# Kernel optimization log

Hardware: AMD Instinct MI355X
Metric: run time of the kernel (lower is better)

The kernel has to match this reference:

```python
import jax, jax.numpy as jnp
import numpy as np

T, B, I, H = 512, 64, 256, 512

def setup_inputs() -> dict:
    key = jax.random.key(0)
    ks = jax.random.split(key, 5)
    s = 0.1  # matches uniform(-0.1, 0.1) init scale
    return {
        "x": jax.random.normal(ks[0], (T, B, I), dtype=jnp.float32),
        "weight_ih": jax.random.uniform(ks[1], (H, I), dtype=jnp.float32, minval=-s, maxval=s),
        "weight_hh": jax.random.uniform(ks[2], (H, H), dtype=jnp.float32, minval=-s, maxval=s),
        "bias_ih": jax.random.uniform(ks[3], (H,), dtype=jnp.float32, minval=-s, maxval=s),
        "bias_hh": jax.random.uniform(ks[4], (H,), dtype=jnp.float32, minval=-s, maxval=s),
    }

def reference(x, weight_ih, weight_hh, bias_ih, bias_hh):
    # Precompute input contribution for all timesteps in one big GEMM: [T,B,H]
    xw = jnp.einsum('tbi,hi->tbh', x, weight_ih) + bias_ih + bias_hh
    h0 = jnp.zeros((x.shape[1], weight_hh.shape[0]), dtype=x.dtype)

    def step(h, xw_t):
        h = jax.nn.relu(xw_t + h @ weight_hh.T)
        return h, h

    h_final, output = jax.lax.scan(step, h0, xw)
    return output, h_final
```

## Files before the change

### kernel.cpp

```cpp
#include <hip/hip_runtime.h>

#define T_DIM 512
#define B_DIM 64
#define I_DIM 256
#define H_DIM 512
#define BH_DIM (B_DIM * H_DIM)


typedef float f32x4_t __attribute__((ext_vector_type(4)));

__device__ __forceinline__ float4 nt_load4(const float4* p) {
  f32x4_t v = __builtin_nontemporal_load((const f32x4_t*)p);
  return make_float4(v.x, v.y, v.z, v.w);
}

__global__ __launch_bounds__(512, 2) void rnn_fused(
    const float* __restrict__ x, const float* __restrict__ wih,
    const float* __restrict__ whh, const float* __restrict__ bih,
    const float* __restrict__ bhh, float* __restrict__ out,
    unsigned long long* __restrict__ stage) {
  __shared__ __align__(16) float4 wihs4[128 * 64];
  __shared__ __align__(16) float hbuf[2][H_DIM];
  __shared__ __align__(16) float4 xbuf4[3 * 64];

  const int b   = blockIdx.x & 63;
  const int rb  = blockIdx.x >> 6;
  const int tid = threadIdx.x;
  const int rg  = tid >> 4;
  const int cg  = tid & 15;
  const int j0  = rb * 128 + rg * 4;

  const int pj = (tid < rb * 128) ? tid : tid + 128;

  float4 w[4][8];
#pragma unroll
  for (int r = 0; r < 4; r++) {
    const float4* wr = (const float4*)(whh + (size_t)(j0 + r) * H_DIM);
#pragma unroll
    for (int i = 0; i < 8; i++) w[r][i] = wr[i * 16 + cg];
  }

  {
    const float4* wg = (const float4*)(wih + (size_t)rb * 128 * I_DIM);
#pragma unroll
    for (int q = 0; q < 16; q++) {
      const int idx = q * 512 + tid;
      wihs4[idx] = wg[idx];
    }
  }

  const float4* xg = (const float4*)x;
  if (tid < 64) {
    xbuf4[0 * 64 + tid] = nt_load4(&xg[((size_t)0 * B_DIM + b) * 64 + tid]);
    xbuf4[1 * 64 + tid] = nt_load4(&xg[((size_t)1 * B_DIM + b) * 64 + tid]);
  }

  float bias = 0.f;
  if (cg < 4) bias = bih[j0 + cg] + bhh[j0 + cg];

  float* __restrict__ outb = out + (size_t)b * H_DIM;
  unsigned long long* __restrict__ stg0 = stage + (size_t)b * H_DIM;
  unsigned long long* __restrict__ stg1 = stage + (size_t)(64 + b) * H_DIM;

  __syncthreads();

  float hlast = 0.f;

  {
    float b0 = 0.f, b1 = 0.f, b2 = 0.f, b3 = 0.f;
    const float4* xb = &xbuf4[0];
    const float4* wr = &wihs4[(rg * 4) * 64];
#pragma unroll
    for (int i = 0; i < 4; i++) {
      const float4 xv = xb[i * 16 + cg];
      const float4 q0 = wr[0 * 64 + i * 16 + cg];
      const float4 q1 = wr[1 * 64 + i * 16 + cg];
      const float4 q2 = wr[2 * 64 + i * 16 + cg];
      const float4 q3 = wr[3 * 64 + i * 16 + cg];
      b0 = fmaf(q0.x, xv.x, b0); b0 = fmaf(q0.y, xv.y, b0);
      b0 = fmaf(q0.z, xv.z, b0); b0 = fmaf(q0.w, xv.w, b0);
      b1 = fmaf(q1.x, xv.x, b1); b1 = fmaf(q1.y, xv.y, b1);
      b1 = fmaf(q1.z, xv.z, b1); b1 = fmaf(q1.w, xv.w, b1);
      b2 = fmaf(q2.x, xv.x, b2); b2 = fmaf(q2.y, xv.y, b2);
      b2 = fmaf(q2.z, xv.z, b2); b2 = fmaf(q2.w, xv.w, b2);
      b3 = fmaf(q3.x, xv.x, b3); b3 = fmaf(q3.y, xv.y, b3);
      b3 = fmaf(q3.z, xv.z, b3); b3 = fmaf(q3.w, xv.w, b3);
    }
#pragma unroll
    for (int m = 1; m <= 8; m <<= 1) {
      b0 += __shfl_xor(b0, m, 64);
      b1 += __shfl_xor(b1, m, 64);
      b2 += __shfl_xor(b2, m, 64);
      b3 += __shfl_xor(b3, m, 64);
    }
    if (cg < 4) {
      const float acc = (cg == 0) ? b0 : (cg == 1) ? b1 : (cg == 2) ? b2 : b3;
      const float h = fmaxf(acc + bias, 0.f);
      const int j = j0 + cg;
      union { float f; unsigned int u; } cv; cv.f = h;
      __hip_atomic_store(&stg0[j], (unsigned long long)cv.u,
                         __ATOMIC_RELAXED, __HIP_MEMORY_SCOPE_AGENT);
      __builtin_nontemporal_store(h, &outb[j]);
      hbuf[0][j] = h;
      hlast = h;
    }
    if (tid < 64) {
      xbuf4[2 * 64 + tid] = nt_load4(&xg[((size_t)2 * B_DIM + b) * 64 + tid]);
    }
  }

  for (int t = 1; t < T_DIM; t++) {
    const int p = (t - 1) & 1;
    float* hb = hbuf[p];
    float* o_t = outb + (size_t)t * BH_DIM;

    float b0 = 0.f, b1 = 0.f, b2 = 0.f, b3 = 0.f;
    {
      const float4* xb = &xbuf4[(t % 3) * 64];
      const float4* wr = &wihs4[(rg * 4) * 64];
#pragma unroll
      for (int i = 0; i < 4; i++) {
        const float4 xv = xb[i * 16 + cg];
        const float4 q0 = wr[0 * 64 + i * 16 + cg];
        const float4 q1 = wr[1 * 64 + i * 16 + cg];
        const float4 q2 = wr[2 * 64 + i * 16 + cg];
        const float4 q3 = wr[3 * 64 + i * 16 + cg];
        b0 = fmaf(q0.x, xv.x, b0); b0 = fmaf(q0.y, xv.y, b0);
        b0 = fmaf(q0.z, xv.z, b0); b0 = fmaf(q0.w, xv.w, b0);
        b1 = fmaf(q1.x, xv.x, b1); b1 = fmaf(q1.y, xv.y, b1);
        b1 = fmaf(q1.z, xv.z, b1); b1 = fmaf(q1.w, xv.w, b1);
        b2 = fmaf(q2.x, xv.x, b2); b2 = fmaf(q2.y, xv.y, b2);
        b2 = fmaf(q2.z, xv.z, b2); b2 = fmaf(q2.w, xv.w, b2);
        b3 = fmaf(q3.x, xv.x, b3); b3 = fmaf(q3.y, xv.y, b3);
        b3 = fmaf(q3.z, xv.z, b3); b3 = fmaf(q3.w, xv.w, b3);
      }
    }

    float4 xpf = make_float4(0.f, 0.f, 0.f, 0.f);
    const bool do_pf = (tid < 64) && (t + 2 < T_DIM);
    if (do_pf) xpf = nt_load4(&xg[((size_t)(t + 2) * B_DIM + b) * 64 + tid]);

    if (tid < 384) {
      unsigned long long* slot = (p ? stg1 : stg0) + pj;
      const unsigned int want = (unsigned int)(t - 1);
      unsigned long long v;
      do {
        v = __hip_atomic_load(slot, __ATOMIC_RELAXED, __HIP_MEMORY_SCOPE_AGENT);
      } while ((unsigned int)(v >> 32) != want);
      union { unsigned int u; float f; } cv; cv.u = (unsigned int)v;
      hb[pj] = cv.f;
    }

    __syncthreads();

    if (do_pf) xbuf4[((t + 2) % 3) * 64 + tid] = xpf;

    float a0 = b0, a1 = b1, a2 = b2, a3 = b3;
#pragma unroll
    for (int i = 0; i < 8; i++) {
      const float4 hv = ((const float4*)hb)[i * 16 + cg];
      a0 = fmaf(w[0][i].x, hv.x, a0); a0 = fmaf(w[0][i].y, hv.y, a0);
      a0 = fmaf(w[0][i].z, hv.z, a0); a0 = fmaf(w[0][i].w, hv.w, a0);
      a1 = fmaf(w[1][i].x, hv.x, a1); a1 = fmaf(w[1][i].y, hv.y, a1);
      a1 = fmaf(w[1][i].z, hv.z, a1); a1 = fmaf(w[1][i].w, hv.w, a1);
      a2 = fmaf(w[2][i].x, hv.x, a2); a2 = fmaf(w[2][i].y, hv.y, a2);
      a2 = fmaf(w[2][i].z, hv.z, a2); a2 = fmaf(w[2][i].w, hv.w, a2);
      a3 = fmaf(w[3][i].x, hv.x, a3); a3 = fmaf(w[3][i].y, hv.y, a3);
      a3 = fmaf(w[3][i].z, hv.z, a3); a3 = fmaf(w[3][i].w, hv.w, a3);
    }
#pragma unroll
    for (int m = 1; m <= 8; m <<= 1) {
      a0 += __shfl_xor(a0, m, 64);
      a1 += __shfl_xor(a1, m, 64);
      a2 += __shfl_xor(a2, m, 64);
      a3 += __shfl_xor(a3, m, 64);
    }

    if (cg < 4) {
      const float acc = (cg == 0) ? a0 : (cg == 1) ? a1 : (cg == 2) ? a2 : a3;
      const float h = fmaxf(acc + bias, 0.f);
      const int j = j0 + cg;
      union { float f; unsigned int u; } cv; cv.f = h;
      const unsigned long long tag = (unsigned long long)(unsigned int)t << 32;
      unsigned long long* sb = (t & 1) ? stg1 : stg0;
      __hip_atomic_store(&sb[j], tag | cv.u,
                         __ATOMIC_RELAXED, __HIP_MEMORY_SCOPE_AGENT);
      __builtin_nontemporal_store(h, &o_t[j]);
      hbuf[t & 1][j] = h;
      hlast = h;
    }
  }

  if (cg < 4) {
    __builtin_nontemporal_store(
        hlast, &out[(size_t)T_DIM * BH_DIM + (size_t)b * H_DIM + j0 + cg]);
  }
}

extern "C" void kernel_launch(void* const* d_in, const int* in_sizes, int n_in,
                              void* d_out, int out_size, void* d_ws, size_t ws_size,
                              hipStream_t stream) {
  const float* x   = (const float*)d_in[0];
  const float* wih = (const float*)d_in[1];
  const float* whh = (const float*)d_in[2];
  const float* bih = (const float*)d_in[3];
  const float* bhh = (const float*)d_in[4];
  float* out = (float*)d_out;
  unsigned long long* stage = (unsigned long long*)d_ws;

  rnn_fused<<<256, 512, 0, stream>>>(x, wih, whh, bih, bhh, out, stage);
}
```

Baseline: 981.1 us.

## Split input projection into a separate GEMM kernel ahead of the recurrent scan

Adds a tiled fp32 GEMM kernel that computes x·W_ih^T plus both biases for all timesteps and writes it into the output buffer. The scan kernel then reads that precomputed value per step instead of doing the input dot-product and x prefetch inside the serial loop, which drops the large W_ih shared-memory tile. The stage tags shift by one so they start at 1, and the shuffle reduction is replaced by DPP row sums. This adds a second launch and an extra read and write of the output tensor in exchange for a shorter per-step critical path.

```diff
diff --git a/kernel.cpp b/kernel.cpp
--- a/kernel.cpp
+++ b/kernel.cpp
@@ -7,21 +7,95 @@
 #define BH_DIM (B_DIM * H_DIM)
 
 
-typedef float f32x4_t __attribute__((ext_vector_type(4)));
-
-__device__ __forceinline__ float4 nt_load4(const float4* p) {
-  f32x4_t v = __builtin_nontemporal_load((const f32x4_t*)p);
-  return make_float4(v.x, v.y, v.z, v.w);
-}
-
-__global__ __launch_bounds__(512, 2) void rnn_fused(
+__global__ __launch_bounds__(256) void xw_gemm(
     const float* __restrict__ x, const float* __restrict__ wih,
-    const float* __restrict__ whh, const float* __restrict__ bih,
-    const float* __restrict__ bhh, float* __restrict__ out,
+    const float* __restrict__ bih, const float* __restrict__ bhh,
+    float* __restrict__ out) {
+  __shared__ __align__(16) float As[32][128];
+  __shared__ __align__(16) float Bs[32][128];
+
+  const int bm = blockIdx.x >> 2;
+  const int bn = blockIdx.x & 3;
+  const int m0 = bm * 128, n0 = bn * 128;
+  const int tid = threadIdx.x;
+  const int tx = tid & 15, ty = tid >> 4;
+  const int ml = tid & 127, kq = tid >> 7;
+
+  float acc[8][8];
+#pragma unroll
+  for (int r = 0; r < 8; r++)
+#pragma unroll
+    for (int c = 0; c < 8; c++) acc[r][c] = 0.f;
+
+  for (int kc = 0; kc < I_DIM; kc += 32) {
+    const float4* xr = (const float4*)(x + (size_t)(m0 + ml) * I_DIM + kc + kq * 16);
+    const float4* br = (const float4*)(wih + (size_t)(n0 + ml) * I_DIM + kc + kq * 16);
+    float4 av[4], bv[4];
+#pragma unroll
+    for (int j = 0; j < 4; j++) { av[j] = xr[j]; bv[j] = br[j]; }
+
+    __syncthreads();
+#pragma unroll
+    for (int j = 0; j < 4; j++) {
+      const int k = kq * 16 + j * 4;
+      As[k + 0][ml] = av[j].x; As[k + 1][ml] = av[j].y;
+      As[k + 2][ml] = av[j].z; As[k + 3][ml] = av[j].w;
+      Bs[k + 0][ml] = bv[j].x; Bs[k + 1][ml] = bv[j].y;
+      Bs[k + 2][ml] = bv[j].z; Bs[k + 3][ml] = bv[j].w;
+    }
+    __syncthreads();
+
+#pragma unroll 4
+    for (int kk = 0; kk < 32; kk++) {
+      const float4 a0 = *(const float4*)&As[kk][ty * 4];
+      const float4 a1 = *(const float4*)&As[kk][64 + ty * 4];
+      const float4 b0 = *(const float4*)&Bs[kk][tx * 4];
+      const float4 b1 = *(const float4*)&Bs[kk][64 + tx * 4];
+      const float ar[8] = {a0.x, a0.y, a0.z, a0.w, a1.x, a1.y, a1.z, a1.w};
+      const float br_[8] = {b0.x, b0.y, b0.z, b0.w, b1.x, b1.y, b1.z, b1.w};
+#pragma unroll
+      for (int r = 0; r < 8; r++)
+#pragma unroll
+        for (int c = 0; c < 8; c++) acc[r][c] = fmaf(ar[r], br_[c], acc[r][c]);
+    }
+  }
+
+  const float4 bi0 = *(const float4*)(bih + n0 + tx * 4);
+  const float4 bh0 = *(const float4*)(bhh + n0 + tx * 4);
+  const float4 bi1 = *(const float4*)(bih + n0 + 64 + tx * 4);
+  const float4 bh1 = *(const float4*)(bhh + n0 + 64 + tx * 4);
+  const float4 bb0 = make_float4(bi0.x + bh0.x, bi0.y + bh0.y, bi0.z + bh0.z, bi0.w + bh0.w);
+  const float4 bb1 = make_float4(bi1.x + bh1.x, bi1.y + bh1.y, bi1.z + bh1.z, bi1.w + bh1.w);
+
+#pragma unroll
+  for (int r = 0; r < 8; r++) {
+    const int m = m0 + ((r < 4) ? (ty * 4 + r) : (64 + ty * 4 + (r - 4)));
+    float4* orow = (float4*)(out + (size_t)m * H_DIM + n0);
+    orow[tx] = make_float4(acc[r][0] + bb0.x, acc[r][1] + bb0.y,
+                           acc[r][2] + bb0.z, acc[r][3] + bb0.w);
+    orow[16 + tx] = make_float4(acc[r][4] + bb1.x, acc[r][5] + bb1.y,
+                                acc[r][6] + bb1.z, acc[r][7] + bb1.w);
+  }
+}
+
+
+__device__ __forceinline__ float row16_sum(float v) {
+  int m;
+  m = __builtin_amdgcn_update_dpp(0, __float_as_int(v), 0xB1, 0xF, 0xF, true);
+  v += __int_as_float(m);
+  m = __builtin_amdgcn_update_dpp(0, __float_as_int(v), 0x4E, 0xF, 0xF, true);
+  v += __int_as_float(m);
+  m = __builtin_amdgcn_update_dpp(0, __float_as_int(v), 0x124, 0xF, 0xF, true);
+  v += __int_as_float(m);
+  m = __builtin_amdgcn_update_dpp(0, __float_as_int(v), 0x128, 0xF, 0xF, true);
+  v += __int_as_float(m);
+  return v;
+}
+
+__global__ __launch_bounds__(512, 2) void rnn_scan(
+    const float* __restrict__ whh, float* __restrict__ out,
     unsigned long long* __restrict__ stage) {
-  __shared__ __align__(16) float4 wihs4[128 * 64];
   __shared__ __align__(16) float hbuf[2][H_DIM];
-  __shared__ __align__(16) float4 xbuf4[3 * 64];
 
   const int b   = blockIdx.x & 63;
   const int rb  = blockIdx.x >> 6;
@@ -40,73 +114,21 @@
     for (int i = 0; i < 8; i++) w[r][i] = wr[i * 16 + cg];
   }
 
-  {
-    const float4* wg = (const float4*)(wih + (size_t)rb * 128 * I_DIM);
-#pragma unroll
-    for (int q = 0; q < 16; q++) {
-      const int idx = q * 512 + tid;
-      wihs4[idx] = wg[idx];
-    }
-  }
-
-  const float4* xg = (const float4*)x;
-  if (tid < 64) {
-    xbuf4[0 * 64 + tid] = nt_load4(&xg[((size_t)0 * B_DIM + b) * 64 + tid]);
-    xbuf4[1 * 64 + tid] = nt_load4(&xg[((size_t)1 * B_DIM + b) * 64 + tid]);
-  }
-
-  float bias = 0.f;
-  if (cg < 4) bias = bih[j0 + cg] + bhh[j0 + cg];
-
   float* __restrict__ outb = out + (size_t)b * H_DIM;
   unsigned long long* __restrict__ stg0 = stage + (size_t)b * H_DIM;
   unsigned long long* __restrict__ stg1 = stage + (size_t)(64 + b) * H_DIM;
 
-  __syncthreads();
-
   float hlast = 0.f;
 
-  {
-    float b0 = 0.f, b1 = 0.f, b2 = 0.f, b3 = 0.f;
-    const float4* xb = &xbuf4[0];
-    const float4* wr = &wihs4[(rg * 4) * 64];
-#pragma unroll
-    for (int i = 0; i < 4; i++) {
-      const float4 xv = xb[i * 16 + cg];
-      const float4 q0 = wr[0 * 64 + i * 16 + cg];
-      const float4 q1 = wr[1 * 64 + i * 16 + cg];
-      const float4 q2 = wr[2 * 64 + i * 16 + cg];
-      const float4 q3 = wr[3 * 64 + i * 16 + cg];
-      b0 = fmaf(q0.x, xv.x, b0); b0 = fmaf(q0.y, xv.y, b0);
-      b0 = fmaf(q0.z, xv.z, b0); b0 = fmaf(q0.w, xv.w, b0);
-      b1 = fmaf(q1.x, xv.x, b1); b1 = fmaf(q1.y, xv.y, b1);
-      b1 = fmaf(q1.z, xv.z, b1); b1 = fmaf(q1.w, xv.w, b1);
-      b2 = fmaf(q2.x, xv.x, b2); b2 = fmaf(q2.y, xv.y, b2);
-      b2 = fmaf(q2.z, xv.z, b2); b2 = fmaf(q2.w, xv.w, b2);
-      b3 = fmaf(q3.x, xv.x, b3); b3 = fmaf(q3.y, xv.y, b3);
-      b3 = fmaf(q3.z, xv.z, b3); b3 = fmaf(q3.w, xv.w, b3);
-    }
-#pragma unroll
-    for (int m = 1; m <= 8; m <<= 1) {
-      b0 += __shfl_xor(b0, m, 64);
-      b1 += __shfl_xor(b1, m, 64);
-      b2 += __shfl_xor(b2, m, 64);
-      b3 += __shfl_xor(b3, m, 64);
-    }
-    if (cg < 4) {
-      const float acc = (cg == 0) ? b0 : (cg == 1) ? b1 : (cg == 2) ? b2 : b3;
-      const float h = fmaxf(acc + bias, 0.f);
-      const int j = j0 + cg;
-      union { float f; unsigned int u; } cv; cv.f = h;
-      __hip_atomic_store(&stg0[j], (unsigned long long)cv.u,
-                         __ATOMIC_RELAXED, __HIP_MEMORY_SCOPE_AGENT);
-      __builtin_nontemporal_store(h, &outb[j]);
-      hbuf[0][j] = h;
-      hlast = h;
-    }
-    if (tid < 64) {
-      xbuf4[2 * 64 + tid] = nt_load4(&xg[((size_t)2 * B_DIM + b) * 64 + tid]);
-    }
+  if (cg < 4) {
+    const int j = j0 + cg;
+    const float h = fmaxf(__builtin_nontemporal_load(&outb[j]), 0.f);
+    union { float f; unsigned int u; } cv; cv.f = h;
+    __hip_atomic_store(&stg0[j], (1ULL << 32) | (unsigned long long)cv.u,
+                       __ATOMIC_RELAXED, __HIP_MEMORY_SCOPE_AGENT);
+    __builtin_nontemporal_store(h, &outb[j]);
+    hbuf[0][j] = h;
+    hlast = h;
   }
 
   for (int t = 1; t < T_DIM; t++) {
@@ -114,35 +136,9 @@
     float* hb = hbuf[p];
     float* o_t = outb + (size_t)t * BH_DIM;
 
-    float b0 = 0.f, b1 = 0.f, b2 = 0.f, b3 = 0.f;
-    {
-      const float4* xb = &xbuf4[(t % 3) * 64];
-      const float4* wr = &wihs4[(rg * 4) * 64];
-#pragma unroll
-      for (int i = 0; i < 4; i++) {
-        const float4 xv = xb[i * 16 + cg];
-        const float4 q0 = wr[0 * 64 + i * 16 + cg];
-        const float4 q1 = wr[1 * 64 + i * 16 + cg];
-        const float4 q2 = wr[2 * 64 + i * 16 + cg];
-        const float4 q3 = wr[3 * 64 + i * 16 + cg];
-        b0 = fmaf(q0.x, xv.x, b0); b0 = fmaf(q0.y, xv.y, b0);
-        b0 = fmaf(q0.z, xv.z, b0); b0 = fmaf(q0.w, xv.w, b0);
-        b1 = fmaf(q1.x, xv.x, b1); b1 = fmaf(q1.y, xv.y, b1);
-        b1 = fmaf(q1.z, xv.z, b1); b1 = fmaf(q1.w, xv.w, b1);
-        b2 = fmaf(q2.x, xv.x, b2); b2 = fmaf(q2.y, xv.y, b2);
-        b2 = fmaf(q2.z, xv.z, b2); b2 = fmaf(q2.w, xv.w, b2);
-        b3 = fmaf(q3.x, xv.x, b3); b3 = fmaf(q3.y, xv.y, b3);
-        b3 = fmaf(q3.z, xv.z, b3); b3 = fmaf(q3.w, xv.w, b3);
-      }
-    }
-
-    float4 xpf = make_float4(0.f, 0.f, 0.f, 0.f);
-    const bool do_pf = (tid < 64) && (t + 2 < T_DIM);
-    if (do_pf) xpf = nt_load4(&xg[((size_t)(t + 2) * B_DIM + b) * 64 + tid]);
-
     if (tid < 384) {
       unsigned long long* slot = (p ? stg1 : stg0) + pj;
-      const unsigned int want = (unsigned int)(t - 1);
+      const unsigned int want = (unsigned int)t;
       unsigned long long v;
       do {
         v = __hip_atomic_load(slot, __ATOMIC_RELAXED, __HIP_MEMORY_SCOPE_AGENT);
@@ -151,11 +147,12 @@
       hb[pj] = cv.f;
     }
 
+    float xwv = 0.f;
+    if (cg < 4) xwv = __builtin_nontemporal_load(&o_t[j0 + cg]);
+
     __syncthreads();
 
-    if (do_pf) xbuf4[((t + 2) % 3) * 64 + tid] = xpf;
-
-    float a0 = b0, a1 = b1, a2 = b2, a3 = b3;
+    float a0 = 0.f, a1 = 0.f, a2 = 0.f, a3 = 0.f;
 #pragma unroll
     for (int i = 0; i < 8; i++) {
       const float4 hv = ((const float4*)hb)[i * 16 + cg];
@@ -168,23 +165,23 @@
       a3 = fmaf(w[3][i].x, hv.x, a3); a3 = fmaf(w[3][i].y, hv.y, a3);
       a3 = fmaf(w[3][i].z, hv.z, a3); a3 = fmaf(w[3][i].w, hv.w, a3);
     }
-#pragma unroll
-    for (int m = 1; m <= 8; m <<= 1) {
-      a0 += __shfl_xor(a0, m, 64);
-      a1 += __shfl_xor(a1, m, 64);
-      a2 += __shfl_xor(a2, m, 64);
-      a3 += __shfl_xor(a3, m, 64);
-    }
+
+    a0 = row16_sum(a0);
+    a1 = row16_sum(a1);
+    a2 = row16_sum(a2);
+    a3 = row16_sum(a3);
 
     if (cg < 4) {
       const float acc = (cg == 0) ? a0 : (cg == 1) ? a1 : (cg == 2) ? a2 : a3;
-      const float h = fmaxf(acc + bias, 0.f);
+      const float h = fmaxf(acc + xwv, 0.f);
       const int j = j0 + cg;
       union { float f; unsigned int u; } cv; cv.f = h;
-      const unsigned long long tag = (unsigned long long)(unsigned int)t << 32;
+      const unsigned long long val =
+          ((unsigned long long)(unsigned int)(t + 1) << 32) |
+          (unsigned long long)cv.u;
       unsigned long long* sb = (t & 1) ? stg1 : stg0;
-      __hip_atomic_store(&sb[j], tag | cv.u,
-                         __ATOMIC_RELAXED, __HIP_MEMORY_SCOPE_AGENT);
+      __hip_atomic_store(&sb[j], val, __ATOMIC_RELAXED,
+                         __HIP_MEMORY_SCOPE_AGENT);
       __builtin_nontemporal_store(h, &o_t[j]);
       hbuf[t & 1][j] = h;
       hlast = h;
@@ -208,5 +205,6 @@
   float* out = (float*)d_out;
   unsigned long long* stage = (unsigned long long*)d_ws;
 
-  rnn_fused<<<256, 512, 0, stream>>>(x, wih, whh, bih, bhh, out, stage);
-}
+  xw_gemm<<<1024, 256, 0, stream>>>(x, wih, bih, bhh, out);
+  rnn_scan<<<256, 512, 0, stream>>>(whh, out, stage);
+}
```

Measured after the change: 887.8 us. 9.5% less time.
